# Kernel tuning notes

Measured on AMD Instinct MI355X. Metric: run time of the kernel, lower is better.

## Reference

```python
import jax, jax.numpy as jnp
import numpy as np

NEG_SLOPE = 0.2


def _gat_layer(x, W, a_src, a_dst, src, dst, ew, num_nodes):
    # Dense projection: [N, Din] @ [Din, Dout] -> [N, Dout]
    h = x @ W
    s = h @ a_src  # per-node source score, [N]
    d = h @ a_dst  # per-node destination score, [N]
    score = jax.nn.leaky_relu(s[src] + d[dst], NEG_SLOPE)  # [E]
    # segment softmax over incoming edges of each destination node
    m = jax.ops.segment_max(score, dst, num_segments=num_nodes)
    ex = jnp.exp(score - m[dst])
    denom = jax.ops.segment_sum(ex, dst, num_segments=num_nodes)
    alpha = ex / jnp.maximum(denom[dst], jnp.asarray(1e-16, ex.dtype))
    alpha = alpha * ew  # edge-weighted attention
    # gather h_j, scale by alpha, scatter-add into destinations
    return jax.ops.segment_sum(h[src] * alpha[:, None], dst, num_segments=num_nodes)


def setup_inputs() -> dict:
    key = jax.random.key(0)
    ks = jax.random.split(key, 9)
    N, E, F_IN, HID, NC = 100000, 1600000, 256, 64, 40
    x = jax.random.normal(ks[0], (N, F_IN), dtype=jnp.float32)
    edge_index = jax.random.randint(ks[1], (2, E), 0, N, dtype=jnp.int32)
    edge_weight = jax.random.uniform(ks[2], (E,), dtype=jnp.float32)
    W1 = jax.random.normal(ks[3], (F_IN, HID), dtype=jnp.float32) / np.sqrt(F_IN)
    a1_src = jax.random.normal(ks[4], (HID,), dtype=jnp.float32) / np.sqrt(HID)
    a1_dst = jax.random.normal(ks[5], (HID,), dtype=jnp.float32) / np.sqrt(HID)
    W2 = jax.random.normal(ks[6], (HID, NC), dtype=jnp.float32) / np.sqrt(HID)
    a2_src = jax.random.normal(ks[7], (NC,), dtype=jnp.float32) / np.sqrt(NC)
    a2_dst = jax.random.normal(ks[8], (NC,), dtype=jnp.float32) / np.sqrt(NC)
    return {"x": x, "edge_index": edge_index, "edge_weight": edge_weight,
            "W1": W1, "a1_src": a1_src, "a1_dst": a1_dst,
            "W2": W2, "a2_src": a2_src, "a2_dst": a2_dst}


def reference(x, edge_index, edge_weight, W1, a1_src, a1_dst, W2, a2_src, a2_dst):
    N = x.shape[0]
    # add_self_loops=True in both convs: append (i, i) edges with weight 1
    loops = jnp.arange(N, dtype=edge_index.dtype)
    src = jnp.concatenate([edge_index[0], loops])
    dst = jnp.concatenate([edge_index[1], loops])
    ew = jnp.concatenate([edge_weight, jnp.ones((N,), edge_weight.dtype)])
    h = jax.nn.relu(_gat_layer(x, W1, a1_src, a1_dst, src, dst, ew, N))
    # dropout inactive in eval mode
    out = _gat_layer(h, W2, a2_src, a2_dst, src, dst, ew, N)
    return out
```

## Files before the change

### kernel.cpp

```cpp
#include <hip/hip_runtime.h>
#include <hip/hip_bf16.h>
#include <math.h>

#define NEG_SLOPE 0.2f

typedef __attribute__((ext_vector_type(4))) float f32x4;
typedef __attribute__((ext_vector_type(8))) short bf16x8;
typedef __attribute__((ext_vector_type(4))) short bf16x4;

__device__ __forceinline__ float leaky(float x) { return x > 0.f ? x : NEG_SLOPE * x; }

__device__ __forceinline__ unsigned short bf_hi(float x) {
  return (unsigned short)(__float_as_uint(x) >> 16);
}

__device__ __forceinline__ unsigned short bf_rne(float x) {
  unsigned u = __float_as_uint(x);
  return (unsigned short)((u + 0x7FFFu + ((u >> 16) & 1u)) >> 16);
}


#define BIN_CHUNK 2048
#define BCAP 8192

__global__ void k_curinit(int* __restrict__ cursor, int NB) {
  int i = blockIdx.x * blockDim.x + threadIdx.x;
  if (i < NB) cursor[i] = i * BCAP;
}

__global__ __launch_bounds__(256)
void k_bin(const int* __restrict__ ei, const float* __restrict__ ew, int E, int N,
           int* __restrict__ cursor, int2* __restrict__ staged, int NB) {
  __shared__ int lhist[512];
  __shared__ int lbase[512];
  int tid = threadIdx.x;
  int start = blockIdx.x * BIN_CHUNK;
  int NT = E + N;
  int srcv[8], dstv[8]; float wv[8];
#pragma unroll
  for (int j = 0; j < 8; j++) {
    int e = start + j * 256 + tid;
    int s = 0, d = -1; float w = 0.f;
    if (e < NT) {
      if (e < E) { s = ei[e]; d = ei[E + e]; w = ew[e]; }
      else       { s = d = e - E; w = 1.f; }
    }
    srcv[j] = s; dstv[j] = d; wv[j] = w;
  }
  for (int b = tid; b < NB; b += 256) lhist[b] = 0;
  __syncthreads();
#pragma unroll
  for (int j = 0; j < 8; j++)
    if (dstv[j] >= 0) atomicAdd(&lhist[dstv[j] >> 8], 1);
  __syncthreads();
  for (int b = tid; b < NB; b += 256) {
    int n = lhist[b];
    lbase[b] = (n > 0) ? atomicAdd(&cursor[b], n) : 0;
    lhist[b] = 0;
  }
  __syncthreads();
#pragma unroll
  for (int j = 0; j < 8; j++) {
    if (dstv[j] >= 0) {
      int bkt = dstv[j] >> 8;
      int off = atomicAdd(&lhist[bkt], 1);
      staged[lbase[bkt] + off] =
          make_int2(srcv[j] | ((dstv[j] & 255) << 24), __float_as_int(wv[j]));
    }
  }
}

__global__ __launch_bounds__(512)
void k_bscan(const int* __restrict__ cursor, int NB, int NT, int N,
             int* __restrict__ bbase, int* __restrict__ rp) {
  __shared__ int sm[512];
  int tid = threadIdx.x;
  int v = (tid < NB) ? cursor[tid] - tid * BCAP : 0;
  sm[tid] = v;
  __syncthreads();
  for (int off = 1; off < 512; off <<= 1) {
    int x = sm[tid];
    int a = (tid >= off) ? sm[tid - off] : 0;
    __syncthreads();
    sm[tid] = x + a;
    __syncthreads();
  }
  if (tid < NB) bbase[tid] = sm[tid] - v;
  if (tid == 0) { bbase[NB] = sm[NB - 1]; rp[N] = NT; }
}

__global__ __launch_bounds__(512)
void k_finalize(const int2* __restrict__ staged, const int* __restrict__ bbase,
                int N, int* __restrict__ rp, int2* __restrict__ csr) {
  __shared__ int cnt[256];
  __shared__ int sm[256];
  int b = blockIdx.x, tid = threadIdx.x;
  int sbase = b * BCAP;
  int cbase = bbase[b];
  int size = bbase[b + 1] - cbase;
  if (tid < 256) cnt[tid] = 0;
  __syncthreads();
  for (int i = tid; i < size; i += 512) {
    int2 v = staged[sbase + i];
    atomicAdd(&cnt[((unsigned)v.x) >> 24], 1);
  }
  __syncthreads();
  int s = 0;
  if (tid < 256) { s = cnt[tid]; sm[tid] = s; }
  __syncthreads();
  for (int off = 1; off < 256; off <<= 1) {
    int x = 0;
    if (tid < 256) { x = sm[tid]; if (tid >= off) x += sm[tid - off]; }
    __syncthreads();
    if (tid < 256) sm[tid] = x;
    __syncthreads();
  }
  if (tid < 256) {
    int excl = sm[tid] - s;
    int node = (b << 8) + tid;
    if (node < N) rp[node] = cbase + excl;
    cnt[tid] = excl;
  }
  __syncthreads();
  for (int i = tid; i < size; i += 512) {
    int2 v = staged[sbase + i];
    int dlow = ((unsigned)v.x) >> 24;
    int pos = cbase + atomicAdd(&cnt[dlow], 1);
    csr[pos] = make_int2(v.x & 0x00FFFFFF, v.y);
  }
}

__global__ __launch_bounds__(256)
void k_wprep(const float* __restrict__ W, int K, int Mout,
             unsigned short* __restrict__ whi, unsigned short* __restrict__ wlo) {
  int idx = blockIdx.x * 256 + threadIdx.x;
  if (idx >= K * 64) return;
  int k = idx >> 6, n = idx & 63;
  float v = (n < Mout) ? W[(size_t)k * Mout + n] : 0.f;
  unsigned short h = bf_hi(v);
  float hf = __uint_as_float((unsigned)h << 16);
  unsigned short l = bf_hi(v - hf);
  int kc = k >> 5, kk = k & 31, quad = kk >> 3, j = kk & 7;
  int ct = n >> 4, nn = n & 15;
  int off = (((kc * 4 + ct) * 64) + quad * 16 + nn) * 8 + j;
  whi[off] = h; wlo[off] = l;
}

__global__ void k_wvec(const float* __restrict__ W2, const float* __restrict__ a2s,
                       const float* __restrict__ a2d, int K, int NC,
                       float* __restrict__ ws, float* __restrict__ wd) {
  int k = threadIdx.x;
  if (k >= K) return;
  float s = 0.f, d = 0.f;
  for (int n = 0; n < NC; n++) {
    float w = W2[(size_t)k * NC + n];
    s += w * a2s[n]; d += w * a2d[n];
  }
  ws[k] = s; wd[k] = d;
}

__global__ __launch_bounds__(256)
void k_gemm_mfma(const float* __restrict__ X, int K,
                 const unsigned short* __restrict__ WHI, const unsigned short* __restrict__ WLO,
                 const float* __restrict__ ASRC, const float* __restrict__ ADST, int Mout,
                 float* __restrict__ Hf, unsigned short* __restrict__ Hb, int ldH,
                 float* __restrict__ S, float* __restrict__ D, int N) {
  __shared__ __align__(16) unsigned short xhi[2048], xlo[2048];
  __shared__ __align__(16) unsigned short whs[2048], wls[2048];
  int tid = threadIdx.x;
  int lane = tid & 63, w = tid >> 6;
  int rowBase = blockIdx.x * 64;

  f32x4 acc[4];
#pragma unroll
  for (int c = 0; c < 4; c++) acc[c] = (f32x4){0.f, 0.f, 0.f, 0.f};

  int q0 = tid, q1 = tid + 256;
  int row0 = q0 >> 3, k40 = (q0 & 7) << 2;
  int row1 = q1 >> 3, k41 = (q1 & 7) << 2;
  int xo0 = (((row0 >> 4) * 64) + (k40 >> 3) * 16 + (row0 & 15)) * 8 + (k40 & 7);
  int xo1 = (((row1 >> 4) * 64) + (k41 >> 3) * 16 + (row1 & 15)) * 8 + (k41 & 7);
  int grow0 = rowBase + row0, grow1 = rowBase + row1;

  int nch = K >> 5;
  f32x4 xr0, xr1; bf16x8 wh, wl;

  xr0 = (f32x4){0.f, 0.f, 0.f, 0.f}; xr1 = xr0;
  if (grow0 < N) xr0 = *(const f32x4*)&X[(size_t)grow0 * K + k40];
  if (grow1 < N) xr1 = *(const f32x4*)&X[(size_t)grow1 * K + k41];
  wh = *(const bf16x8*)(WHI + tid * 8);
  wl = *(const bf16x8*)(WLO + tid * 8);

  for (int kc = 0; kc < nch; kc++) {
    bf16x4 h4, l4;
#pragma unroll
    for (int i = 0; i < 4; i++) {
      unsigned short h = bf_hi(xr0[i]);
      float hf = __uint_as_float((unsigned)h << 16);
      h4[i] = (short)h; l4[i] = (short)bf_hi(xr0[i] - hf);
    }
    *(bf16x4*)(xhi + xo0) = h4; *(bf16x4*)(xlo + xo0) = l4;
#pragma unroll
    for (int i = 0; i < 4; i++) {
      unsigned short h = bf_hi(xr1[i]);
      float hf = __uint_as_float((unsigned)h << 16);
      h4[i] = (short)h; l4[i] = (short)bf_hi(xr1[i] - hf);
    }
    *(bf16x4*)(xhi + xo1) = h4; *(bf16x4*)(xlo + xo1) = l4;
    *(bf16x8*)(whs + tid * 8) = wh;
    *(bf16x8*)(wls + tid * 8) = wl;
    __syncthreads();

    if (kc + 1 < nch) {
      int kb = (kc + 1) << 5;
      xr0 = (f32x4){0.f, 0.f, 0.f, 0.f}; xr1 = xr0;
      if (grow0 < N) xr0 = *(const f32x4*)&X[(size_t)grow0 * K + kb + k40];
      if (grow1 < N) xr1 = *(const f32x4*)&X[(size_t)grow1 * K + kb + k41];
      wh = *(const bf16x8*)(WHI + (size_t)(kc + 1) * 2048 + tid * 8);
      wl = *(const bf16x8*)(WLO + (size_t)(kc + 1) * 2048 + tid * 8);
    }

    bf16x8 ah = *(const bf16x8*)(xhi + (w * 64 + lane) * 8);
    bf16x8 al = *(const bf16x8*)(xlo + (w * 64 + lane) * 8);
#pragma unroll
    for (int c = 0; c < 4; c++) {
      bf16x8 bh = *(const bf16x8*)(whs + (c * 64 + lane) * 8);
      bf16x8 bl = *(const bf16x8*)(wls + (c * 64 + lane) * 8);
      acc[c] = __builtin_amdgcn_mfma_f32_16x16x32_bf16(ah, bh, acc[c], 0, 0, 0);
      acc[c] = __builtin_amdgcn_mfma_f32_16x16x32_bf16(ah, bl, acc[c], 0, 0, 0);
      acc[c] = __builtin_amdgcn_mfma_f32_16x16x32_bf16(al, bh, acc[c], 0, 0, 0);
    }
    __syncthreads();
  }

  int nn = lane & 15, quad = lane >> 4;
  float as_[4], ad_[4];
#pragma unroll
  for (int c = 0; c < 4; c++) {
    int col = c * 16 + nn;
    as_[c] = (col < Mout) ? ASRC[col] : 0.f;
    ad_[c] = (col < Mout) ? ADST[col] : 0.f;
  }
#pragma unroll
  for (int r = 0; r < 4; r++) {
    int grow = rowBase + w * 16 + quad * 4 + r;
    float ps = 0.f, pd = 0.f;
#pragma unroll
    for (int c = 0; c < 4; c++) {
      float v = acc[c][r];
      int col = c * 16 + nn;
      if (grow < N && col < Mout) {
        if (Hb) Hb[(size_t)grow * ldH + col] = bf_rne(v);
        else    Hf[(size_t)grow * ldH + col] = v;
      }
      ps += v * as_[c]; pd += v * ad_[c];
    }
#pragma unroll
    for (int off = 1; off < 16; off <<= 1) {
      ps += __shfl_xor(ps, off);
      pd += __shfl_xor(pd, off);
    }
    if (nn == 0 && grow < N) { S[grow] = ps; D[grow] = pd; }
  }
}

template <bool OUTB16, bool RELU, bool SCORES>
__global__ __launch_bounds__(256)
void k_agg(const int* __restrict__ rp, const int2* __restrict__ csr,
           const float* __restrict__ S, const float* __restrict__ D,
           const unsigned short* __restrict__ Hb, void* __restrict__ OutV,
           const float* __restrict__ WS, const float* __restrict__ WD,
           float* __restrict__ S2, float* __restrict__ D2, int N) {
  int gw = (blockIdx.x * blockDim.x + threadIdx.x) >> 6;
  int lane = threadIdx.x & 63;
  int sub = lane >> 4, fl = lane & 15;
  int node = gw * 4 + sub;
  bool active = node < N;
  int b = 0, e = 1; float dd = 0.f;
  if (active) { b = rp[node]; e = rp[node + 1]; dd = D[node]; }
  float den = 0.f;
  f32x4 acc0 = (f32x4){0.f, 0.f, 0.f, 0.f};
  f32x4 acc1 = (f32x4){0.f, 0.f, 0.f, 0.f};

  int need = e - b;
  need = max(need, __shfl_xor(need, 16));
  need = max(need, __shfl_xor(need, 32));
  int iters = (need + 3) >> 2;
  int last = e - 1;

  int idx[4]; float wgt[4];
  int t = b;
#pragma unroll
  for (int j = 0; j < 4; j++) {
    int tj = (t + j < e) ? t + j : last;
    int2 p = csr[tj];
    idx[j] = p.x;
    wgt[j] = (t + j < e) ? __int_as_float(p.y) : 0.f;
  }

  for (int it = 0; it < iters; it++, t += 4) {
    float sv[4];
#pragma unroll
    for (int j = 0; j < 4; j++) sv[j] = S[idx[j]];
    f32x4 hv[4];
#pragma unroll
    for (int j = 0; j < 4; j++) {
      ushort4 uv = *(const ushort4*)(Hb + (size_t)idx[j] * 64 + (fl << 2));
      hv[j][0] = __uint_as_float((unsigned)uv.x << 16);
      hv[j][1] = __uint_as_float((unsigned)uv.y << 16);
      hv[j][2] = __uint_as_float((unsigned)uv.z << 16);
      hv[j][3] = __uint_as_float((unsigned)uv.w << 16);
    }
    int idn[4]; float wgn[4];
#pragma unroll
    for (int j = 0; j < 4; j++) {
      int tj = (t + 4 + j < e) ? t + 4 + j : last;
      int2 p = csr[tj];
      idn[j] = p.x;
      wgn[j] = (t + 4 + j < e) ? __int_as_float(p.y) : 0.f;
    }
    float ex[4];
#pragma unroll
    for (int j = 0; j < 4; j++)
      ex[j] = (t + j < e) ? __expf(leaky(sv[j] + dd)) : 0.f;
    den += (ex[0] + ex[1]) + (ex[2] + ex[3]);
    acc0 += hv[0] * (ex[0] * wgt[0]) + hv[1] * (ex[1] * wgt[1]);
    acc1 += hv[2] * (ex[2] * wgt[2]) + hv[3] * (ex[3] * wgt[3]);
#pragma unroll
    for (int j = 0; j < 4; j++) { idx[j] = idn[j]; wgt[j] = wgn[j]; }
  }

  float inv = 1.0f / fmaxf(den, 1e-16f);
  f32x4 o = (acc0 + acc1) * inv;
  if (RELU) {
#pragma unroll
    for (int j = 0; j < 4; j++) o[j] = fmaxf(o[j], 0.f);
  }
  if (SCORES) {
    f32x4 ws = *(const f32x4*)&WS[fl << 2];
    f32x4 wd = *(const f32x4*)&WD[fl << 2];
    float ps = o[0] * ws[0] + o[1] * ws[1] + o[2] * ws[2] + o[3] * ws[3];
    float pd = o[0] * wd[0] + o[1] * wd[1] + o[2] * wd[2] + o[3] * wd[3];
#pragma unroll
    for (int off = 1; off < 16; off <<= 1) {
      ps += __shfl_xor(ps, off);
      pd += __shfl_xor(pd, off);
    }
    if (active && fl == 0) { S2[node] = ps; D2[node] = pd; }
  }
  if (active) {
    if (OUTB16) {
      ushort4 st;
      st.x = bf_rne(o[0]); st.y = bf_rne(o[1]); st.z = bf_rne(o[2]); st.w = bf_rne(o[3]);
      *(ushort4*)((unsigned short*)OutV + (size_t)node * 64 + (fl << 2)) = st;
    } else {
      *(f32x4*)((float*)OutV + (size_t)node * 64 + (fl << 2)) = o;
    }
  }
}

extern "C" void kernel_launch(void* const* d_in, const int* in_sizes, int n_in,
                              void* d_out, int out_size, void* d_ws, size_t ws_size,
                              hipStream_t stream) {
  const float* x   = (const float*)d_in[0];
  const int*   ei  = (const int*)d_in[1];
  const float* ew  = (const float*)d_in[2];
  const float* W1  = (const float*)d_in[3];
  const float* a1s = (const float*)d_in[4];
  const float* a1d = (const float*)d_in[5];
  const float* W2  = (const float*)d_in[6];
  const float* a2s = (const float*)d_in[7];
  const float* a2d = (const float*)d_in[8];

  const int HID = in_sizes[4];
  const int NC  = in_sizes[7];
  const int FIN = in_sizes[3] / HID;
  const int N   = in_sizes[0] / FIN;
  const int E   = in_sizes[2];
  const int NT  = E + N;
  const int NB  = (N + 255) >> 8;
  float* out = (float*)d_out;

  char* wsb = (char*)d_ws;
  size_t off = 0;
  auto alloc = [&](size_t bytes) -> char* {
    char* p = wsb + off;
    off += (bytes + 255) & ~(size_t)255;
    return p;
  };
  unsigned short* h1b = (unsigned short*)alloc((size_t)N * 64 * 2);
  unsigned short* h2b = (unsigned short*)alloc((size_t)N * 64 * 2);
  float* A      = (float*)alloc((size_t)N * 64 * 4);
  float* S      = (float*)alloc((size_t)N * 4);
  float* D      = (float*)alloc((size_t)N * 4);
  float* S2     = (float*)alloc((size_t)N * 4);
  float* D2     = (float*)alloc((size_t)N * 4);
  int*   rp     = (int*)alloc((size_t)(N + 1) * 4);
  int*   bbase  = (int*)alloc((size_t)(NB + 1) * 4);
  int*   cursor = (int*)alloc((size_t)NB * 4);
  int2*  csr    = (int2*)alloc((size_t)NT * 8);
  int2*  staged = (int2*)alloc((size_t)NB * BCAP * 8);
  unsigned short* whi1 = (unsigned short*)alloc((size_t)FIN * 64 * 2);
  unsigned short* wlo1 = (unsigned short*)alloc((size_t)FIN * 64 * 2);
  unsigned short* whi2 = (unsigned short*)alloc((size_t)HID * 64 * 2);
  unsigned short* wlo2 = (unsigned short*)alloc((size_t)HID * 64 * 2);
  float* w2s = (float*)alloc((size_t)HID * 4);
  float* w2d = (float*)alloc((size_t)HID * 4);
  (void)ws_size; (void)n_in; (void)out_size;

  const int ebins = (NT + BIN_CHUNK - 1) / BIN_CHUNK;

  hipLaunchKernelGGL(k_curinit, dim3((NB + 255) / 256), dim3(256), 0, stream, cursor, NB);
  hipLaunchKernelGGL(k_bin, dim3(ebins), dim3(256), 0, stream, ei, ew, E, N, cursor, staged, NB);
  hipLaunchKernelGGL(k_bscan, dim3(1), dim3(512), 0, stream, cursor, NB, NT, N, bbase, rp);
  hipLaunchKernelGGL(k_finalize, dim3(NB), dim3(512), 0, stream, staged, bbase, N, rp, csr);

  hipLaunchKernelGGL(k_wprep, dim3((FIN * 64 + 255) / 256), dim3(256), 0, stream,
                     W1, FIN, HID, whi1, wlo1);
  hipLaunchKernelGGL(k_wprep, dim3((HID * 64 + 255) / 256), dim3(256), 0, stream,
                     W2, HID, NC, whi2, wlo2);
  hipLaunchKernelGGL(k_wvec, dim3(1), dim3(64), 0, stream, W2, a2s, a2d, HID, NC, w2s, w2d);

  const int gblocks = (N + 63) / 64;
  const int ablocks = (N + 15) / 16;

  hipLaunchKernelGGL(k_gemm_mfma, dim3(gblocks), dim3(256), 0, stream,
                     x, FIN, whi1, wlo1, a1s, a1d, HID, (float*)nullptr, h1b, 64, S, D, N);
  hipLaunchKernelGGL((k_agg<true, true, true>), dim3(ablocks), dim3(256), 0, stream,
                     rp, csr, S, D, h1b, (void*)h2b, w2s, w2d, S2, D2, N);
  hipLaunchKernelGGL((k_agg<false, false, false>), dim3(ablocks), dim3(256), 0, stream,
                     rp, csr, S2, D2, h2b, (void*)A, (const float*)nullptr,
                     (const float*)nullptr, (float*)nullptr, (float*)nullptr, N);
  hipLaunchKernelGGL(k_gemm_mfma, dim3(gblocks), dim3(256), 0, stream,
                     A, HID, whi2, wlo2, a2s, a2d, NC, out, (unsigned short*)nullptr, NC, S, D, N);
}
```

Before: 356.7 us.

## Fold layer-1 attention coefficients into CSR finalize and deepen agg gather prefetch

The CSR finalize kernel now runs after the first GEMM, so as it scatters edges it can compute the layer-1 edge exp scores and per-destination denominators. It writes a second CSR copy whose weights are the precomputed ex*w, so the first aggregation skips the S gathers and the exp. The aggregation loop also now prefetches the bf16 feature rows one group of four edges ahead, in addition to the index prefetch. The cost is an extra 8-byte-per-edge CSR array written and kept, plus shared-memory float atomics for the denominators, and the finalize can no longer overlap with the GEMM.

Measured after the change: 383.0 us. +7.4%, slower.

```diff
diff --git a/kernel.cpp b/kernel.cpp
--- a/kernel.cpp
+++ b/kernel.cpp
@@ -91,14 +91,22 @@
 
 __global__ __launch_bounds__(512)
 void k_finalize(const int2* __restrict__ staged, const int* __restrict__ bbase,
-                int N, int* __restrict__ rp, int2* __restrict__ csr) {
+                const float* __restrict__ S, const float* __restrict__ D, int N,
+                int* __restrict__ rp, int2* __restrict__ csrA, int2* __restrict__ csrB,
+                float* __restrict__ DEN) {
   __shared__ int cnt[256];
   __shared__ int sm[256];
+  __shared__ float dl[256];
+  __shared__ float denl[256];
   int b = blockIdx.x, tid = threadIdx.x;
   int sbase = b * BCAP;
   int cbase = bbase[b];
   int size = bbase[b + 1] - cbase;
-  if (tid < 256) cnt[tid] = 0;
+  if (tid < 256) {
+    cnt[tid] = 0; denl[tid] = 0.f;
+    int node = (b << 8) + tid;
+    dl[tid] = (node < N) ? D[node] : 0.f;
+  }
   __syncthreads();
   for (int i = tid; i < size; i += 512) {
     int2 v = staged[sbase + i];
@@ -125,8 +133,18 @@
   for (int i = tid; i < size; i += 512) {
     int2 v = staged[sbase + i];
     int dlow = ((unsigned)v.x) >> 24;
+    int src = v.x & 0x00FFFFFF;
     int pos = cbase + atomicAdd(&cnt[dlow], 1);
-    csr[pos] = make_int2(v.x & 0x00FFFFFF, v.y);
+    float w = __int_as_float(v.y);
+    float ex = __expf(leaky(S[src] + dl[dlow]));
+    csrB[pos] = make_int2(src, v.y);
+    csrA[pos] = make_int2(src, __float_as_int(ex * w));
+    atomicAdd(&denl[dlow], ex);
+  }
+  __syncthreads();
+  if (tid < 256) {
+    int node = (b << 8) + tid;
+    if (node < N) DEN[node] = denl[tid];
   }
 }
 
@@ -264,11 +282,12 @@
   }
 }
 
-template <bool OUTB16, bool RELU, bool SCORES>
+template <bool COEF, bool OUTB16, bool RELU, bool SCORES>
 __global__ __launch_bounds__(256)
 void k_agg(const int* __restrict__ rp, const int2* __restrict__ csr,
-           const float* __restrict__ S, const float* __restrict__ D,
-           const unsigned short* __restrict__ Hb, void* __restrict__ OutV,
+           const float* __restrict__ Sc, const float* __restrict__ Dc,
+           const float* __restrict__ DEN, const unsigned short* __restrict__ Hb,
+           void* __restrict__ OutV,
            const float* __restrict__ WS, const float* __restrict__ WD,
            float* __restrict__ S2, float* __restrict__ D2, int N) {
   int gw = (blockIdx.x * blockDim.x + threadIdx.x) >> 6;
@@ -276,8 +295,12 @@
   int sub = lane >> 4, fl = lane & 15;
   int node = gw * 4 + sub;
   bool active = node < N;
-  int b = 0, e = 1; float dd = 0.f;
-  if (active) { b = rp[node]; e = rp[node + 1]; dd = D[node]; }
+  int b = 0, e = 1; float dd = 0.f, dpre = 1.f;
+  if (active) {
+    b = rp[node]; e = rp[node + 1];
+    if (COEF) dpre = DEN[node];
+    else      dd = Dc[node];
+  }
   float den = 0.f;
   f32x4 acc0 = (f32x4){0.f, 0.f, 0.f, 0.f};
   f32x4 acc1 = (f32x4){0.f, 0.f, 0.f, 0.f};
@@ -288,49 +311,81 @@
   int iters = (need + 3) >> 2;
   int last = e - 1;
 
-  int idx[4]; float wgt[4];
+  int idx0[4], idx1[4]; float w0[4], w1[4];
+#pragma unroll
+  for (int j = 0; j < 4; j++) {
+    int tj = (b + j < e) ? b + j : last;
+    int2 p = csr[tj];
+    idx0[j] = p.x; w0[j] = (b + j < e) ? __int_as_float(p.y) : 0.f;
+  }
+#pragma unroll
+  for (int j = 0; j < 4; j++) {
+    int tj = (b + 4 + j < e) ? b + 4 + j : last;
+    int2 p = csr[tj];
+    idx1[j] = p.x; w1[j] = (b + 4 + j < e) ? __int_as_float(p.y) : 0.f;
+  }
+  ushort4 u0[4];
+#pragma unroll
+  for (int j = 0; j < 4; j++)
+    u0[j] = *(const ushort4*)(Hb + (size_t)idx0[j] * 64 + (fl << 2));
+  float sv0[4];
+  if (!COEF) {
+#pragma unroll
+    for (int j = 0; j < 4; j++) sv0[j] = Sc[idx0[j]];
+  }
+
   int t = b;
-#pragma unroll
-  for (int j = 0; j < 4; j++) {
-    int tj = (t + j < e) ? t + j : last;
-    int2 p = csr[tj];
-    idx[j] = p.x;
-    wgt[j] = (t + j < e) ? __int_as_float(p.y) : 0.f;
-  }
-
   for (int it = 0; it < iters; it++, t += 4) {
-    float sv[4];
-#pragma unroll
-    for (int j = 0; j < 4; j++) sv[j] = S[idx[j]];
+    ushort4 u1[4];
+#pragma unroll
+    for (int j = 0; j < 4; j++)
+      u1[j] = *(const ushort4*)(Hb + (size_t)idx1[j] * 64 + (fl << 2));
+    float sv1[4];
+    if (!COEF) {
+#pragma unroll
+      for (int j = 0; j < 4; j++) sv1[j] = Sc[idx1[j]];
+    }
+    int idx2[4]; float w2[4];
+#pragma unroll
+    for (int j = 0; j < 4; j++) {
+      int tj = (t + 8 + j < e) ? t + 8 + j : last;
+      int2 p = csr[tj];
+      idx2[j] = p.x; w2[j] = (t + 8 + j < e) ? __int_as_float(p.y) : 0.f;
+    }
+    float cf[4];
+    if (COEF) {
+#pragma unroll
+      for (int j = 0; j < 4; j++) cf[j] = w0[j];
+    } else {
+      float ex[4];
+#pragma unroll
+      for (int j = 0; j < 4; j++)
+        ex[j] = (t + j < e) ? __expf(leaky(sv0[j] + dd)) : 0.f;
+      den += (ex[0] + ex[1]) + (ex[2] + ex[3]);
+#pragma unroll
+      for (int j = 0; j < 4; j++) cf[j] = ex[j] * w0[j];
+    }
     f32x4 hv[4];
 #pragma unroll
     for (int j = 0; j < 4; j++) {
-      ushort4 uv = *(const ushort4*)(Hb + (size_t)idx[j] * 64 + (fl << 2));
-      hv[j][0] = __uint_as_float((unsigned)uv.x << 16);
-      hv[j][1] = __uint_as_float((unsigned)uv.y << 16);
-      hv[j][2] = __uint_as_float((unsigned)uv.z << 16);
-      hv[j][3] = __uint_as_float((unsigned)uv.w << 16);
-    }
-    int idn[4]; float wgn[4];
+      hv[j][0] = __uint_as_float((unsigned)u0[j].x << 16);
+      hv[j][1] = __uint_as_float((unsigned)u0[j].y << 16);
+      hv[j][2] = __uint_as_float((unsigned)u0[j].z << 16);
+      hv[j][3] = __uint_as_float((unsigned)u0[j].w << 16);
+    }
+    acc0 += hv[0] * cf[0] + hv[1] * cf[1];
+    acc1 += hv[2] * cf[2] + hv[3] * cf[3];
 #pragma unroll
     for (int j = 0; j < 4; j++) {
-      int tj = (t + 4 + j < e) ? t + 4 + j : last;
-      int2 p = csr[tj];
-      idn[j] = p.x;
-      wgn[j] = (t + 4 + j < e) ? __int_as_float(p.y) : 0.f;
-    }
-    float ex[4];
-#pragma unroll
-    for (int j = 0; j < 4; j++)
-      ex[j] = (t + j < e) ? __expf(leaky(sv[j] + dd)) : 0.f;
-    den += (ex[0] + ex[1]) + (ex[2] + ex[3]);
-    acc0 += hv[0] * (ex[0] * wgt[0]) + hv[1] * (ex[1] * wgt[1]);
-    acc1 += hv[2] * (ex[2] * wgt[2]) + hv[3] * (ex[3] * wgt[3]);
-#pragma unroll
-    for (int j = 0; j < 4; j++) { idx[j] = idn[j]; wgt[j] = wgn[j]; }
-  }
-
-  float inv = 1.0f / fmaxf(den, 1e-16f);
+      idx0[j] = idx1[j]; w0[j] = w1[j];
+      idx1[j] = idx2[j]; w1[j] = w2[j];
+      u0[j] = u1[j];
+      if (!COEF) sv0[j] = sv1[j];
+    }
+  }
+
+  float dv = COEF ? dpre : den;
+  float inv = 1.0f / fmaxf(dv, 1e-16f);
   f32x4 o = (acc0 + acc1) * inv;
   if (RELU) {
 #pragma unroll
@@ -395,10 +450,12 @@
   float* D      = (float*)alloc((size_t)N * 4);
   float* S2     = (float*)alloc((size_t)N * 4);
   float* D2     = (float*)alloc((size_t)N * 4);
+  float* DEN    = (float*)alloc((size_t)N * 4);
   int*   rp     = (int*)alloc((size_t)(N + 1) * 4);
   int*   bbase  = (int*)alloc((size_t)(NB + 1) * 4);
   int*   cursor = (int*)alloc((size_t)NB * 4);
-  int2*  csr    = (int2*)alloc((size_t)NT * 8);
+  int2*  csrA   = (int2*)alloc((size_t)NT * 8);
+  int2*  csrB   = (int2*)alloc((size_t)NT * 8);
   int2*  staged = (int2*)alloc((size_t)NB * BCAP * 8);
   unsigned short* whi1 = (unsigned short*)alloc((size_t)FIN * 64 * 2);
   unsigned short* wlo1 = (unsigned short*)alloc((size_t)FIN * 64 * 2);
@@ -409,28 +466,31 @@
   (void)ws_size; (void)n_in; (void)out_size;
 
   const int ebins = (NT + BIN_CHUNK - 1) / BIN_CHUNK;
+  const int gblocks = (N + 63) / 64;
+  const int ablocks = (N + 15) / 16;
 
   hipLaunchKernelGGL(k_curinit, dim3((NB + 255) / 256), dim3(256), 0, stream, cursor, NB);
   hipLaunchKernelGGL(k_bin, dim3(ebins), dim3(256), 0, stream, ei, ew, E, N, cursor, staged, NB);
   hipLaunchKernelGGL(k_bscan, dim3(1), dim3(512), 0, stream, cursor, NB, NT, N, bbase, rp);
-  hipLaunchKernelGGL(k_finalize, dim3(NB), dim3(512), 0, stream, staged, bbase, N, rp, csr);
 
   hipLaunchKernelGGL(k_wprep, dim3((FIN * 64 + 255) / 256), dim3(256), 0, stream,
                      W1, FIN, HID, whi1, wlo1);
   hipLaunchKernelGGL(k_wprep, dim3((HID * 64 + 255) / 256), dim3(256), 0, stream,
                      W2, HID, NC, whi2, wlo2);
   hipLaunchKernelGGL(k_wvec, dim3(1), dim3(64), 0, stream, W2, a2s, a2d, HID, NC, w2s, w2d);
-
-  const int gblocks = (N + 63) / 64;
-  const int ablocks = (N + 15) / 16;
-
   hipLaunchKernelGGL(k_gemm_mfma, dim3(gblocks), dim3(256), 0, stream,
                      x, FIN, whi1, wlo1, a1s, a1d, HID, (float*)nullptr, h1b, 64, S, D, N);
-  hipLaunchKernelGGL((k_agg<true, true, true>), dim3(ablocks), dim3(256), 0, stream,
-                     rp, csr, S, D, h1b, (void*)h2b, w2s, w2d, S2, D2, N);
-  hipLaunchKernelGGL((k_agg<false, false, false>), dim3(ablocks), dim3(256), 0, stream,
-                     rp, csr, S2, D2, h2b, (void*)A, (const float*)nullptr,
-                     (const float*)nullptr, (float*)nullptr, (float*)nullptr, N);
+
+  hipLaunchKernelGGL(k_finalize, dim3(NB), dim3(512), 0, stream,
+                     staged, bbase, S, D, N, rp, csrA, csrB, DEN);
+
+  hipLaunchKernelGGL((k_agg<true, true, true, true>), dim3(ablocks), dim3(256), 0, stream,
+                     rp, csrA, (const float*)nullptr, (const float*)nullptr, DEN,
+                     h1b, (void*)h2b, w2s, w2d, S2, D2, N);
+  hipLaunchKernelGGL((k_agg<false, false, false, false>), dim3(ablocks), dim3(256), 0, stream,
+                     rp, csrB, S2, D2, (const float*)nullptr,
+                     h2b, (void*)A, (const float*)nullptr, (const float*)nullptr,
+                     (float*)nullptr, (float*)nullptr, N);
   hipLaunchKernelGGL(k_gemm_mfma, dim3(gblocks), dim3(256), 0, stream,
                      A, HID, whi2, wlo2, a2s, a2d, NC, out, (unsigned short*)nullptr, NC, S, D, N);
 }
```

## Fold layer-1 attention coefficients into CSR build and merge prep kernels

Applied to the files above, without the earlier changes.

The first GEMM now runs before the edge binning pass. The binning kernel gathers per-edge source and destination scores, computes the exponentiated attention weight times the edge weight, and accumulates each destination's denominator with global atomics. The finalize step writes a second CSR whose payload is that precomputed coefficient, so the layer-1 aggregation skips the per-edge score gather and exp. The weight-prep kernels are merged into one launch. In exchange it adds 1.7M random score gathers and float atomics in binning, extra staged and CSR buffers, and makes the denominator's summation order nondeterministic.

New measurement: 452.7 us. +26.9%, slower.

```diff
diff --git a/kernel.cpp b/kernel.cpp
--- a/kernel.cpp
+++ b/kernel.cpp
@@ -23,14 +23,17 @@
 #define BIN_CHUNK 2048
 #define BCAP 8192
 
-__global__ void k_curinit(int* __restrict__ cursor, int NB) {
+__global__ void k_curinit(int* __restrict__ cursor, int NB, float* __restrict__ DEN, int N) {
   int i = blockIdx.x * blockDim.x + threadIdx.x;
   if (i < NB) cursor[i] = i * BCAP;
+  if (i < N) DEN[i] = 0.f;
 }
 
 __global__ __launch_bounds__(256)
 void k_bin(const int* __restrict__ ei, const float* __restrict__ ew, int E, int N,
-           int* __restrict__ cursor, int2* __restrict__ staged, int NB) {
+           const float* __restrict__ S, const float* __restrict__ D,
+           int* __restrict__ cursor, int2* __restrict__ staged,
+           float* __restrict__ stagedEx, float* __restrict__ DEN, int NB) {
   __shared__ int lhist[512];
   __shared__ int lbase[512];
   int tid = threadIdx.x;
@@ -47,6 +50,13 @@
     }
     srcv[j] = s; dstv[j] = d; wv[j] = w;
   }
+  float sg[8], dg[8];
+#pragma unroll
+  for (int j = 0; j < 8; j++) {
+    int si = (dstv[j] >= 0) ? srcv[j] : 0;
+    int di = (dstv[j] >= 0) ? dstv[j] : 0;
+    sg[j] = S[si]; dg[j] = D[di];
+  }
   for (int b = tid; b < NB; b += 256) lhist[b] = 0;
   __syncthreads();
 #pragma unroll
@@ -59,13 +69,18 @@
     lhist[b] = 0;
   }
   __syncthreads();
+  float exv[8];
+#pragma unroll
+  for (int j = 0; j < 8; j++) exv[j] = __expf(leaky(sg[j] + dg[j]));
 #pragma unroll
   for (int j = 0; j < 8; j++) {
     if (dstv[j] >= 0) {
       int bkt = dstv[j] >> 8;
       int off = atomicAdd(&lhist[bkt], 1);
-      staged[lbase[bkt] + off] =
-          make_int2(srcv[j] | ((dstv[j] & 255) << 24), __float_as_int(wv[j]));
+      int pos = lbase[bkt] + off;
+      staged[pos] = make_int2(srcv[j] | ((dstv[j] & 255) << 24), __float_as_int(wv[j]));
+      stagedEx[pos] = exv[j] * wv[j];
+      atomicAdd(&DEN[dstv[j]], exv[j]);
     }
   }
 }
@@ -90,8 +105,9 @@
 }
 
 __global__ __launch_bounds__(512)
-void k_finalize(const int2* __restrict__ staged, const int* __restrict__ bbase,
-                int N, int* __restrict__ rp, int2* __restrict__ csr) {
+void k_finalize(const int2* __restrict__ staged, const float* __restrict__ stagedEx,
+                const int* __restrict__ bbase, int N, int* __restrict__ rp,
+                int2* __restrict__ csrA, int2* __restrict__ csrB) {
   __shared__ int cnt[256];
   __shared__ int sm[256];
   int b = blockIdx.x, tid = threadIdx.x;
@@ -124,17 +140,18 @@
   __syncthreads();
   for (int i = tid; i < size; i += 512) {
     int2 v = staged[sbase + i];
+    float exw = stagedEx[sbase + i];
     int dlow = ((unsigned)v.x) >> 24;
+    int src = v.x & 0x00FFFFFF;
     int pos = cbase + atomicAdd(&cnt[dlow], 1);
-    csr[pos] = make_int2(v.x & 0x00FFFFFF, v.y);
-  }
-}
-
-__global__ __launch_bounds__(256)
-void k_wprep(const float* __restrict__ W, int K, int Mout,
-             unsigned short* __restrict__ whi, unsigned short* __restrict__ wlo) {
-  int idx = blockIdx.x * 256 + threadIdx.x;
-  if (idx >= K * 64) return;
+    csrB[pos] = make_int2(src, v.y);
+    csrA[pos] = make_int2(src, __float_as_int(exw));
+  }
+}
+
+__device__ __forceinline__ void wprep_one(const float* __restrict__ W, int idx, int Mout,
+                                          unsigned short* __restrict__ whi,
+                                          unsigned short* __restrict__ wlo) {
   int k = idx >> 6, n = idx & 63;
   float v = (n < Mout) ? W[(size_t)k * Mout + n] : 0.f;
   unsigned short h = bf_hi(v);
@@ -146,17 +163,30 @@
   whi[off] = h; wlo[off] = l;
 }
 
-__global__ void k_wvec(const float* __restrict__ W2, const float* __restrict__ a2s,
-                       const float* __restrict__ a2d, int K, int NC,
-                       float* __restrict__ ws, float* __restrict__ wd) {
-  int k = threadIdx.x;
-  if (k >= K) return;
-  float s = 0.f, d = 0.f;
-  for (int n = 0; n < NC; n++) {
-    float w = W2[(size_t)k * NC + n];
-    s += w * a2s[n]; d += w * a2d[n];
-  }
-  ws[k] = s; wd[k] = d;
+__global__ __launch_bounds__(256)
+void k_prep(const float* __restrict__ W1, const float* __restrict__ W2,
+            const float* __restrict__ a2s, const float* __restrict__ a2d,
+            int FIN, int HID, int NC,
+            unsigned short* __restrict__ whi1, unsigned short* __restrict__ wlo1,
+            unsigned short* __restrict__ whi2, unsigned short* __restrict__ wlo2,
+            float* __restrict__ w2s, float* __restrict__ w2d) {
+  int blk = blockIdx.x, tid = threadIdx.x;
+  int nb1 = (FIN * 64) >> 8;
+  int nb2 = (HID * 64) >> 8;
+  if (blk < nb1) {
+    wprep_one(W1, blk * 256 + tid, HID, whi1, wlo1);
+  } else if (blk < nb1 + nb2) {
+    wprep_one(W2, (blk - nb1) * 256 + tid, NC, whi2, wlo2);
+  } else {
+    if (tid < HID) {
+      float s = 0.f, d = 0.f;
+      for (int n = 0; n < NC; n++) {
+        float w = W2[(size_t)tid * NC + n];
+        s += w * a2s[n]; d += w * a2d[n];
+      }
+      w2s[tid] = s; w2d[tid] = d;
+    }
+  }
 }
 
 __global__ __launch_bounds__(256)
@@ -264,11 +294,12 @@
   }
 }
 
-template <bool OUTB16, bool RELU, bool SCORES>
+template <bool COEF, bool OUTB16, bool RELU, bool SCORES>
 __global__ __launch_bounds__(256)
 void k_agg(const int* __restrict__ rp, const int2* __restrict__ csr,
-           const float* __restrict__ S, const float* __restrict__ D,
-           const unsigned short* __restrict__ Hb, void* __restrict__ OutV,
+           const float* __restrict__ Sc, const float* __restrict__ Dc,
+           const float* __restrict__ DEN, const unsigned short* __restrict__ Hb,
+           void* __restrict__ OutV,
            const float* __restrict__ WS, const float* __restrict__ WD,
            float* __restrict__ S2, float* __restrict__ D2, int N) {
   int gw = (blockIdx.x * blockDim.x + threadIdx.x) >> 6;
@@ -276,8 +307,12 @@
   int sub = lane >> 4, fl = lane & 15;
   int node = gw * 4 + sub;
   bool active = node < N;
-  int b = 0, e = 1; float dd = 0.f;
-  if (active) { b = rp[node]; e = rp[node + 1]; dd = D[node]; }
+  int b = 0, e = 1; float dd = 0.f, dpre = 1.f;
+  if (active) {
+    b = rp[node]; e = rp[node + 1];
+    if (COEF) dpre = DEN[node];
+    else      dd = Dc[node];
+  }
   float den = 0.f;
   f32x4 acc0 = (f32x4){0.f, 0.f, 0.f, 0.f};
   f32x4 acc1 = (f32x4){0.f, 0.f, 0.f, 0.f};
@@ -300,8 +335,10 @@
 
   for (int it = 0; it < iters; it++, t += 4) {
     float sv[4];
-#pragma unroll
-    for (int j = 0; j < 4; j++) sv[j] = S[idx[j]];
+    if (!COEF) {
+#pragma unroll
+      for (int j = 0; j < 4; j++) sv[j] = Sc[idx[j]];
+    }
     f32x4 hv[4];
 #pragma unroll
     for (int j = 0; j < 4; j++) {
@@ -319,18 +356,27 @@
       idn[j] = p.x;
       wgn[j] = (t + 4 + j < e) ? __int_as_float(p.y) : 0.f;
     }
-    float ex[4];
-#pragma unroll
-    for (int j = 0; j < 4; j++)
-      ex[j] = (t + j < e) ? __expf(leaky(sv[j] + dd)) : 0.f;
-    den += (ex[0] + ex[1]) + (ex[2] + ex[3]);
-    acc0 += hv[0] * (ex[0] * wgt[0]) + hv[1] * (ex[1] * wgt[1]);
-    acc1 += hv[2] * (ex[2] * wgt[2]) + hv[3] * (ex[3] * wgt[3]);
+    float cf[4];
+    if (COEF) {
+#pragma unroll
+      for (int j = 0; j < 4; j++) cf[j] = wgt[j];
+    } else {
+      float ex[4];
+#pragma unroll
+      for (int j = 0; j < 4; j++)
+        ex[j] = (t + j < e) ? __expf(leaky(sv[j] + dd)) : 0.f;
+      den += (ex[0] + ex[1]) + (ex[2] + ex[3]);
+#pragma unroll
+      for (int j = 0; j < 4; j++) cf[j] = ex[j] * wgt[j];
+    }
+    acc0 += hv[0] * cf[0] + hv[1] * cf[1];
+    acc1 += hv[2] * cf[2] + hv[3] * cf[3];
 #pragma unroll
     for (int j = 0; j < 4; j++) { idx[j] = idn[j]; wgt[j] = wgn[j]; }
   }
 
-  float inv = 1.0f / fmaxf(den, 1e-16f);
+  float dv = COEF ? dpre : den;
+  float inv = 1.0f / fmaxf(dv, 1e-16f);
   f32x4 o = (acc0 + acc1) * inv;
   if (RELU) {
 #pragma unroll
@@ -395,11 +441,14 @@
   float* D      = (float*)alloc((size_t)N * 4);
   float* S2     = (float*)alloc((size_t)N * 4);
   float* D2     = (float*)alloc((size_t)N * 4);
+  float* DEN    = (float*)alloc((size_t)N * 4);
   int*   rp     = (int*)alloc((size_t)(N + 1) * 4);
   int*   bbase  = (int*)alloc((size_t)(NB + 1) * 4);
   int*   cursor = (int*)alloc((size_t)NB * 4);
-  int2*  csr    = (int2*)alloc((size_t)NT * 8);
+  int2*  csrA   = (int2*)alloc((size_t)NT * 8);
+  int2*  csrB   = (int2*)alloc((size_t)NT * 8);
   int2*  staged = (int2*)alloc((size_t)NB * BCAP * 8);
+  float* stagedEx = (float*)alloc((size_t)NB * BCAP * 4);
   unsigned short* whi1 = (unsigned short*)alloc((size_t)FIN * 64 * 2);
   unsigned short* wlo1 = (unsigned short*)alloc((size_t)FIN * 64 * 2);
   unsigned short* whi2 = (unsigned short*)alloc((size_t)HID * 64 * 2);
@@ -409,28 +458,30 @@
   (void)ws_size; (void)n_in; (void)out_size;
 
   const int ebins = (NT + BIN_CHUNK - 1) / BIN_CHUNK;
-
-  hipLaunchKernelGGL(k_curinit, dim3((NB + 255) / 256), dim3(256), 0, stream, cursor, NB);
-  hipLaunchKernelGGL(k_bin, dim3(ebins), dim3(256), 0, stream, ei, ew, E, N, cursor, staged, NB);
-  hipLaunchKernelGGL(k_bscan, dim3(1), dim3(512), 0, stream, cursor, NB, NT, N, bbase, rp);
-  hipLaunchKernelGGL(k_finalize, dim3(NB), dim3(512), 0, stream, staged, bbase, N, rp, csr);
-
-  hipLaunchKernelGGL(k_wprep, dim3((FIN * 64 + 255) / 256), dim3(256), 0, stream,
-                     W1, FIN, HID, whi1, wlo1);
-  hipLaunchKernelGGL(k_wprep, dim3((HID * 64 + 255) / 256), dim3(256), 0, stream,
-                     W2, HID, NC, whi2, wlo2);
-  hipLaunchKernelGGL(k_wvec, dim3(1), dim3(64), 0, stream, W2, a2s, a2d, HID, NC, w2s, w2d);
-
   const int gblocks = (N + 63) / 64;
   const int ablocks = (N + 15) / 16;
-
+  const int nprep = ((FIN * 64) >> 8) + ((HID * 64) >> 8) + 1;
+
+  hipLaunchKernelGGL(k_curinit, dim3((N + 255) / 256), dim3(256), 0, stream,
+                     cursor, NB, DEN, N);
+  hipLaunchKernelGGL(k_prep, dim3(nprep), dim3(256), 0, stream,
+                     W1, W2, a2s, a2d, FIN, HID, NC,
+                     whi1, wlo1, whi2, wlo2, w2s, w2d);
   hipLaunchKernelGGL(k_gemm_mfma, dim3(gblocks), dim3(256), 0, stream,
                      x, FIN, whi1, wlo1, a1s, a1d, HID, (float*)nullptr, h1b, 64, S, D, N);
-  hipLaunchKernelGGL((k_agg<true, true, true>), dim3(ablocks), dim3(256), 0, stream,
-                     rp, csr, S, D, h1b, (void*)h2b, w2s, w2d, S2, D2, N);
-  hipLaunchKernelGGL((k_agg<false, false, false>), dim3(ablocks), dim3(256), 0, stream,
-                     rp, csr, S2, D2, h2b, (void*)A, (const float*)nullptr,
-                     (const float*)nullptr, (float*)nullptr, (float*)nullptr, N);
+  hipLaunchKernelGGL(k_bin, dim3(ebins), dim3(256), 0, stream,
+                     ei, ew, E, N, S, D, cursor, staged, stagedEx, DEN, NB);
+  hipLaunchKernelGGL(k_bscan, dim3(1), dim3(512), 0, stream, cursor, NB, NT, N, bbase, rp);
+  hipLaunchKernelGGL(k_finalize, dim3(NB), dim3(512), 0, stream,
+                     staged, stagedEx, bbase, N, rp, csrA, csrB);
+
+  hipLaunchKernelGGL((k_agg<true, true, true, true>), dim3(ablocks), dim3(256), 0, stream,
+                     rp, csrA, (const float*)nullptr, (const float*)nullptr, DEN,
+                     h1b, (void*)h2b, w2s, w2d, S2, D2, N);
+  hipLaunchKernelGGL((k_agg<false, false, false, false>), dim3(ablocks), dim3(256), 0, stream,
+                     rp, csrB, S2, D2, (const float*)nullptr,
+                     h2b, (void*)A, (const float*)nullptr, (const float*)nullptr,
+                     (float*)nullptr, (float*)nullptr, N);
   hipLaunchKernelGGL(k_gemm_mfma, dim3(gblocks), dim3(256), 0, stream,
                      A, HID, whi2, wlo2, a2s, a2d, NC, out, (unsigned short*)nullptr, NC, S, D, N);
 }
```
